# Kernel optimization log

Hardware: AMD Instinct MI355X
Metric: run time of the kernel (lower is better)

The kernel has to match this reference:

```python
import jax, jax.numpy as jnp
import numpy as np

N, CH, H, W = 2, 64, 96, 96
NH, CHUNK, RED = 4, 144, 4
CM = CH // RED  # match channels = 16
RES_SCALE = 1.0
NORM_EPS = 5e-5


def conv2d(x, w, b):
    # 3x3 'same' conv, NCHW / OIHW
    y = jax.lax.conv_general_dilated(x, w, (1, 1), 'SAME',
                                     dimension_numbers=('NCHW', 'OIHW', 'NCHW'))
    return y + b[None, :, None, None]


def setup_inputs() -> dict:
    key = jax.random.key(0)
    ks = jax.random.split(key, 8)
    L = H * W
    hb = min(L // CHUNK + (L // CHUNK) % 2, 128)  # = 64
    x = jax.random.normal(ks[0], (N, CH, H, W), jnp.float32)
    # per-round semi-orthogonal rotations: rows of (CM, hb) orthonormal
    g = jax.random.normal(ks[1], (NH, hb, CM), jnp.float32)
    q = jnp.stack([jnp.linalg.qr(g[h])[0] for h in range(NH)])  # (NH, hb, CM)
    rot = jnp.transpose(q, (2, 0, 1))  # (CM, NH, hb)
    def s(k, shape, fan):
        return jax.random.normal(k, shape, jnp.float32) / np.sqrt(fan).astype(np.float32)
    wm = s(ks[2], (CM, CH, 3, 3), CH * 9)
    wa = s(ks[3], (CH, CH, 3, 3), CH * 9)
    wf = s(ks[4], (CH, CH, 3, 3), CH * 9)
    fc1_w = s(ks[5], (CHUNK, CH), CH)
    fc2_w = s(ks[6], (CHUNK, CHUNK), CHUNK)
    return {'x': x, 'rot': rot,
            'wm': wm, 'bm': jnp.zeros((CM,), jnp.float32),
            'wa': wa, 'ba': jnp.zeros((CH,), jnp.float32),
            'wf': wf, 'bf': jnp.zeros((CH,), jnp.float32),
            'fc1_w': fc1_w, 'fc1_b': jnp.zeros((CHUNK,), jnp.float32),
            'fc2_w': fc2_w, 'fc2_b': jnp.zeros((CHUNK,), jnp.float32)}


def reference(x, rot, wm, bm, wa, ba, wf, bf, fc1_w, fc1_b, fc2_w, fc2_b):
    n, _, h, w = x.shape
    L = h * w
    hb = rot.shape[-1]
    # embeddings: (N, L, C)
    xe = jax.nn.relu(conv2d(x, wm, bm)).reshape(n, CM, L).transpose(0, 2, 1)
    ye = jax.nn.relu(conv2d(x, wa, ba)).reshape(n, CH, L).transpose(0, 2, 1)
    fe = jax.nn.relu(conv2d(x, wf, bf)).reshape(n, CH, L).transpose(0, 2, 1)
    # LSH: argmax over rotated directions, offset per round (detached in original)
    rv = jnp.einsum('ntf,fhi->nhti', xe, rot)  # (N, NH, L, hb)
    codes = jnp.argmax(rv, -1) + (jnp.arange(NH) * hb)[None, :, None]
    codes = codes.reshape(n, NH * L)
    idx = jnp.argsort(codes, axis=-1)
    undo = jnp.argsort(idx, axis=-1)
    mod = idx % L
    gather = lambda t: jnp.take_along_axis(t, mod[..., None], axis=1)
    nch = L // CHUNK  # L chosen divisible by CHUNK -> padding = 0
    xs = gather(xe).reshape(n, NH, nch, CHUNK, CM)
    ys = gather(ye).reshape(n, NH, nch, CHUNK, CH)
    fs = gather(fe).reshape(n, NH, nch, CHUNK, CH)
    nrm = jnp.linalg.norm(xs, axis=-1, keepdims=True)
    xmatch = xs / jnp.maximum(nrm, NORM_EPS)
    adj = lambda t: jnp.concatenate([t, jnp.roll(t, 1, axis=2), jnp.roll(t, -1, axis=2)], axis=3)
    xmatch = adj(xmatch)   # (n, NH, nch, 3*CHUNK, CM)
    ya = adj(ys)           # (n, NH, nch, 3*CHUNK, CH)
    fa = adj(fs)           # (n, NH, nch, 3*CHUNK, CH)
    hid = jax.nn.relu(fa @ fc1_w.T + fc1_b)
    fc_raw = jnp.swapaxes(hid @ fc2_w.T + fc2_b, -1, -2)  # (n, NH, nch, CHUNK, 3*CHUNK)
    raw = jnp.einsum('nhkie,nhkje->nhkij', xs, xmatch) + fc_raw
    bsc = jax.scipy.special.logsumexp(raw, axis=-1, keepdims=True)
    score = jnp.exp(raw - bsc)
    ret = jnp.einsum('nhkij,nhkje->nhkie', score, ya)  # (n, NH, nch, CHUNK, CH)
    ret = ret.reshape(n, NH * L, CH)
    bsc = bsc.reshape(n, NH * L)
    ret = jnp.take_along_axis(ret, undo[..., None], axis=1)
    bsc = jnp.take_along_axis(bsc, undo, axis=1)
    ret = ret.reshape(n, NH, L, CH)
    probs = jax.nn.softmax(bsc.reshape(n, NH, L, 1), axis=1)
    out = jnp.sum(ret * probs, axis=1)  # (n, L, CH)
    out = out.transpose(0, 2, 1).reshape(n, CH, h, w)
    return out * RES_SCALE + x
```

## Files before the change

kernel.cpp:

```cpp
#include <hip/hip_runtime.h>
#include <hip/hip_bf16.h>

#define LL 9216
#define TOT 36864
#define CHK 144
#define NSEG 144
#define EPS_N 5e-5f

typedef __bf16 bf16x8 __attribute__((ext_vector_type(8)));
typedef float f32x4 __attribute__((ext_vector_type(4)));

__device__ __forceinline__ float dot4(float4 a, float4 b) {
    return a.x*b.x + a.y*b.y + a.z*b.z + a.w*b.w;
}
__device__ __forceinline__ unsigned short f2bf(float f) {
    __hip_bfloat16 h = __float2bfloat16(f);
    return *reinterpret_cast<unsigned short*>(&h);
}
__device__ __forceinline__ float bf2f(unsigned short u) {
    return __uint_as_float(((unsigned int)u) << 16);
}

__global__ __launch_bounds__(256) void k_front(
    const float* __restrict__ x, const float* __restrict__ wm,
    const float* __restrict__ bm, const float* __restrict__ rot,
    unsigned short* __restrict__ xeb, unsigned short* __restrict__ xnb,
    unsigned char* __restrict__ codes,
    const float* __restrict__ fc1w, const float* __restrict__ fc2w,
    const float* __restrict__ wa, const float* __restrict__ wf,
    unsigned short* __restrict__ w1bf, unsigned short* __restrict__ w2bf,
    unsigned short* __restrict__ wpack)
{
    int tid = threadIdx.x;
    if (blockIdx.x >= 288) {
        int i = (blockIdx.x - 288) * 256 + tid;
        if (i < 144 * 64) w1bf[i] = f2bf(fc1w[i]);
        if (i < 144 * 160) {
            int r = i / 160, c = i - r * 160;
            w2bf[i] = (c < 144) ? f2bf(fc2w[r * 144 + c]) : 0;
        }
        if (i < 128 * 576) {
            int o = i / 576, kk = i - o * 576;
            int dydx = kk >> 6, c = kk & 63;
            const float* src = (o < 64) ? wa : wf;
            wpack[i] = f2bf(src[(o & 63) * 576 + c * 9 + dydx]);
        }
        return;
    }
    __shared__ float xl[6400];
    __shared__ float rotT[4096];
    __shared__ float xsp[64 * 20];
    int b = blockIdx.x;
    int n = b / 144, tile = b % 144;
    int ty0 = (tile / 12) * 8, tx0 = (tile % 12) * 8;
    for (int li = tid; li < 6400; li += 256) {
        int c = li / 100, s = li % 100;
        int yy = s / 10, xx = s % 10;
        int gy = ty0 + yy - 1, gx = tx0 + xx - 1;
        float v = 0.f;
        if ((unsigned)gy < 96u && (unsigned)gx < 96u)
            v = x[((n * 64 + c) * 96 + gy) * 96 + gx];
        xl[li] = v;
    }
    for (int e = tid; e < 4096; e += 256) {
        int f = e >> 8, r = e & 255;
        rotT[r * 16 + f] = rot[f * 256 + r];
    }
    __syncthreads();
    int p = tid & 63, og = tid >> 6;
    int row = p >> 3, col = p & 7;
    int ogs = __builtin_amdgcn_readfirstlane(og);
    const float* wb = wm + (size_t)ogs * 4 * 576;
    float acc0 = 0.f, acc1 = 0.f, acc2 = 0.f, acc3 = 0.f;
    for (int c = 0; c < 64; ++c) {
        float xp[9];
        int base = c * 100 + row * 10 + col;
        #pragma unroll
        for (int dy = 0; dy < 3; ++dy)
            #pragma unroll
            for (int dx = 0; dx < 3; ++dx)
                xp[dy * 3 + dx] = xl[base + dy * 10 + dx];
        const float* w0 = wb + c * 9;
        #pragma unroll
        for (int u = 0; u < 9; ++u) {
            acc0 += w0[u]        * xp[u];
            acc1 += w0[576 + u]  * xp[u];
            acc2 += w0[1152 + u] * xp[u];
            acc3 += w0[1728 + u] * xp[u];
        }
    }
    int o = ogs * 4;
    float v0 = acc0 + bm[o + 0]; v0 = v0 > 0.f ? v0 : 0.f;
    float v1 = acc1 + bm[o + 1]; v1 = v1 > 0.f ? v1 : 0.f;
    float v2 = acc2 + bm[o + 2]; v2 = v2 > 0.f ? v2 : 0.f;
    float v3 = acc3 + bm[o + 3]; v3 = v3 > 0.f ? v3 : 0.f;
    size_t t = (size_t)n * LL + (ty0 + row) * 96 + tx0 + col;
    unsigned short pk[4] = {f2bf(v0), f2bf(v1), f2bf(v2), f2bf(v3)};
    *(uint2*)(xeb + t * 16 + o) = *(uint2*)pk;
    *(float4*)(xsp + p * 20 + o) = make_float4(v0, v1, v2, v3);
    __syncthreads();
    int pos = tid & 63, h = tid >> 6;
    int prow = pos >> 3, pcol = pos & 7;
    size_t tc = (size_t)n * LL + (ty0 + prow) * 96 + tx0 + pcol;
    float4 q0 = *(float4*)(xsp + pos * 20 + 0);
    float4 q1 = *(float4*)(xsp + pos * 20 + 4);
    float4 q2 = *(float4*)(xsp + pos * 20 + 8);
    float4 q3 = *(float4*)(xsp + pos * 20 + 12);
    if (h == 0) {
        float nn = dot4(q0,q0) + dot4(q1,q1) + dot4(q2,q2) + dot4(q3,q3);
        float s = fmaxf(sqrtf(nn), EPS_N);
        float inv = 1.f / s;
        unsigned short pn[16];
        pn[0]=f2bf(q0.x*inv);  pn[1]=f2bf(q0.y*inv);  pn[2]=f2bf(q0.z*inv);  pn[3]=f2bf(q0.w*inv);
        pn[4]=f2bf(q1.x*inv);  pn[5]=f2bf(q1.y*inv);  pn[6]=f2bf(q1.z*inv);  pn[7]=f2bf(q1.w*inv);
        pn[8]=f2bf(q2.x*inv);  pn[9]=f2bf(q2.y*inv);  pn[10]=f2bf(q2.z*inv); pn[11]=f2bf(q2.w*inv);
        pn[12]=f2bf(q3.x*inv); pn[13]=f2bf(q3.y*inv); pn[14]=f2bf(q3.z*inv); pn[15]=f2bf(q3.w*inv);
        *(uint4*)(xnb + tc * 16)     = ((uint4*)pn)[0];
        *(uint4*)(xnb + tc * 16 + 8) = ((uint4*)pn)[1];
    }
    float best = -1e30f; int bi = 0;
    const float* rp = rotT + h * 1024;
    for (int i = 0; i < 64; ++i) {
        const float4* r4 = (const float4*)(rp + i * 16);
        float v = dot4(q0, r4[0]) + dot4(q1, r4[1]) + dot4(q2, r4[2]) + dot4(q3, r4[3]);
        if (v > best) { best = v; bi = i; }
    }
    codes[(size_t)n * TOT + h * LL + (tc - (size_t)n * LL)] = (unsigned char)(h * 64 + bi);
}

__global__ __launch_bounds__(256) void k_convbf_fc(
    const float* __restrict__ x, const unsigned short* __restrict__ wpack,
    const float* __restrict__ ba, const float* __restrict__ bfb,
    const unsigned short* __restrict__ w1bf, const float* __restrict__ fc1_b,
    const unsigned short* __restrict__ w2bf, const float* __restrict__ fc2_b,
    unsigned short* __restrict__ yeb, unsigned short* __restrict__ re2b,
    const unsigned char* __restrict__ codes, int* __restrict__ hist)
{
    __shared__ unsigned short xt[3 * 50 * 72];
    __shared__ unsigned short fet[48 * 72];
    __shared__ unsigned short hb [48 * 168];
    __shared__ int lh[256];
    int tid = threadIdx.x;
    if (blockIdx.x >= 384) {
        int b2 = blockIdx.x - 384;
        int n = b2 / NSEG, seg = b2 % NSEG;
        lh[tid] = 0;
        __syncthreads();
        int code = codes[(size_t)n * TOT + seg * 256 + tid];
        atomicAdd(&lh[code], 1);
        __syncthreads();
        hist[((size_t)n * 256 + tid) * NSEG + seg] = lh[tid];
        return;
    }
    int b = blockIdx.x;
    int n = b / 192, rem = b % 192;
    int y = rem >> 1, strip = rem & 1;
    int x0 = strip * 48;
    for (int e = tid; e < 9600; e += 256) {
        int r = e / 3200, r2 = e - r * 3200;
        int c = r2 / 50, j = r2 - c * 50;
        int gy = y - 1 + r, gx = x0 - 1 + j;
        float v = 0.f;
        if ((unsigned)gy < 96u && (unsigned)gx < 96u)
            v = x[((n * 64 + c) * 96 + gy) * 96 + gx];
        xt[(r * 50 + j) * 72 + c] = f2bf(v);
    }
    for (int e = tid; e < 384; e += 256) {
        int r = e >> 3, pq = e & 7;
        *(unsigned int*)(hb + r * 168 + 144 + pq * 2) = 0;
    }
    __syncthreads();
    int wave = tid >> 6, lane = tid & 63;
    int n16 = lane & 15, quad = lane >> 4;
    f32x4 acc[2][3];
    #pragma unroll
    for (int mi = 0; mi < 2; ++mi)
        #pragma unroll
        for (int nt = 0; nt < 3; ++nt) acc[mi][nt] = (f32x4){0.f, 0.f, 0.f, 0.f};
    #pragma unroll
    for (int s = 0; s < 18; ++s) {
        int dydx = s >> 1, half = s & 1;
        int dy = dydx / 3, dxm = dydx - dy * 3;
        bf16x8 B[3];
        #pragma unroll
        for (int nt = 0; nt < 3; ++nt) {
            int j = nt * 16 + n16 + dxm;
            B[nt] = *(bf16x8*)(xt + (dy * 50 + j) * 72 + half * 32 + quad * 8);
        }
        #pragma unroll
        for (int mi = 0; mi < 2; ++mi) {
            int o = (wave * 2 + mi) * 16 + n16;
            bf16x8 A = *(const bf16x8*)(wpack + o * 576 + dydx * 64 + half * 32 + quad * 8);
            #pragma unroll
            for (int nt = 0; nt < 3; ++nt)
                acc[mi][nt] = __builtin_amdgcn_mfma_f32_16x16x32_bf16(A, B[nt], acc[mi][nt], 0, 0, 0);
        }
    }
    #pragma unroll
    for (int mi = 0; mi < 2; ++mi) {
        int mt = wave * 2 + mi;
        int obase = mt * 16 + quad * 4;
        float4 b4 = (mt < 4) ? *(const float4*)(ba + obase)
                             : *(const float4*)(bfb + obase - 64);
        #pragma unroll
        for (int nt = 0; nt < 3; ++nt) {
            int j = nt * 16 + n16;
            unsigned short pk[4];
            float v0 = acc[mi][nt][0] + b4.x; pk[0] = f2bf(v0 > 0.f ? v0 : 0.f);
            float v1 = acc[mi][nt][1] + b4.y; pk[1] = f2bf(v1 > 0.f ? v1 : 0.f);
            float v2 = acc[mi][nt][2] + b4.z; pk[2] = f2bf(v2 > 0.f ? v2 : 0.f);
            float v3 = acc[mi][nt][3] + b4.w; pk[3] = f2bf(v3 > 0.f ? v3 : 0.f);
            if (mt < 4) {
                size_t t = (size_t)n * LL + y * 96 + x0 + j;
                *(uint2*)(yeb + t * 64 + obase) = *(uint2*)pk;
            } else {
                *(uint2*)(fet + j * 72 + (obase - 64)) = *(uint2*)pk;
            }
        }
    }
    __syncthreads();
    size_t R0 = (size_t)n * LL + y * 96 + x0;
    for (int nt = wave; nt < 9; nt += 4) {
        int bn = nt * 16 + n16;
        bf16x8 b0 = *(const bf16x8*)(w1bf + bn * 64 + quad * 8);
        bf16x8 b1 = *(const bf16x8*)(w1bf + bn * 64 + 32 + quad * 8);
        float bb = fc1_b[bn];
        #pragma unroll
        for (int m = 0; m < 3; ++m) {
            int arow = m * 16 + n16;
            bf16x8 a0 = *(bf16x8*)(fet + arow * 72 + quad * 8);
            bf16x8 a1 = *(bf16x8*)(fet + arow * 72 + 32 + quad * 8);
            f32x4 c2 = {0.f, 0.f, 0.f, 0.f};
            c2 = __builtin_amdgcn_mfma_f32_16x16x32_bf16(a0, b0, c2, 0, 0, 0);
            c2 = __builtin_amdgcn_mfma_f32_16x16x32_bf16(a1, b1, c2, 0, 0, 0);
            #pragma unroll
            for (int r = 0; r < 4; ++r) {
                float v = c2[r] + bb;
                hb[(m * 16 + quad * 4 + r) * 168 + bn] = f2bf(v > 0.f ? v : 0.f);
            }
        }
    }
    __syncthreads();
    for (int nt = wave; nt < 9; nt += 4) {
        int bn = nt * 16 + n16;
        bf16x8 wv2[5];
        #pragma unroll
        for (int kk = 0; kk < 5; ++kk)
            wv2[kk] = *(const bf16x8*)(w2bf + bn * 160 + kk * 32 + quad * 8);
        float bb = fc2_b[bn];
        #pragma unroll
        for (int m = 0; m < 3; ++m) {
            int arow = m * 16 + n16;
            f32x4 c2 = {0.f, 0.f, 0.f, 0.f};
            #pragma unroll
            for (int kk = 0; kk < 5; ++kk) {
                bf16x8 a = *(bf16x8*)(hb + arow * 168 + kk * 32 + quad * 8);
                c2 = __builtin_amdgcn_mfma_f32_16x16x32_bf16(a, wv2[kk], c2, 0, 0, 0);
            }
            #pragma unroll
            for (int r = 0; r < 4; ++r)
                re2b[(R0 + m * 16 + quad * 4 + r) * 144 + bn] = f2bf(c2[r] + bb);
        }
    }
}

__global__ void k_scan(int* __restrict__ hist)
{
    __shared__ int sc[256];
    int n = blockIdx.x, bin = threadIdx.x;
    int* hp = hist + ((size_t)n * 256 + bin) * NSEG;
    int4 buf[36];
    int4* hp4 = (int4*)hp;
    #pragma unroll
    for (int q = 0; q < 36; ++q) buf[q] = hp4[q];
    int running = 0;
    #pragma unroll
    for (int q = 0; q < 36; ++q) {
        int t0 = buf[q].x; buf[q].x = running; running += t0;
        int t1 = buf[q].y; buf[q].y = running; running += t1;
        int t2 = buf[q].z; buf[q].z = running; running += t2;
        int t3 = buf[q].w; buf[q].w = running; running += t3;
    }
    sc[bin] = running;
    __syncthreads();
    for (int off = 1; off < 256; off <<= 1) {
        int v = sc[bin];
        int u = (bin >= off) ? sc[bin - off] : 0;
        __syncthreads();
        sc[bin] = v + u;
        __syncthreads();
    }
    int bs = sc[bin] - running;
    #pragma unroll
    for (int q = 0; q < 36; ++q) {
        buf[q].x += bs; buf[q].y += bs; buf[q].z += bs; buf[q].w += bs;
        hp4[q] = buf[q];
    }
}

__global__ __launch_bounds__(256) void k_place(
    const unsigned char* __restrict__ codes, const int* __restrict__ hist,
    int* __restrict__ idx)
{
    __shared__ unsigned char cl[256];
    int b = blockIdx.x, n = b / NSEG, seg = b % NSEG;
    int tid = threadIdx.x;
    int my = codes[(size_t)n * TOT + seg * 256 + tid];
    cl[tid] = (unsigned char)my;
    __syncthreads();
    int rank = 0;
    for (int j = 0; j < tid; ++j) rank += (cl[j] == my);
    int pos = hist[((size_t)n * 256 + my) * NSEG + seg] + rank;
    idx[(size_t)n * TOT + pos] = seg * 256 + tid;
}

__global__ __launch_bounds__(256) void k_gather(
    const int* __restrict__ idx, const unsigned short* __restrict__ xeb,
    const unsigned short* __restrict__ xnb, const unsigned short* __restrict__ yeb,
    const unsigned short* __restrict__ re2b,
    unsigned short* __restrict__ qs, unsigned short* __restrict__ ks,
    unsigned short* __restrict__ vsT, unsigned short* __restrict__ fst,
    int* __restrict__ undo)
{
    __shared__ int tl[144];
    int b0 = blockIdx.x;
    int b = ((b0 & 7) << 6) | (b0 >> 3);
    int nh = b >> 6, chunk = b & 63;
    int n = nh >> 2, h = nh & 3;
    size_t gb = (size_t)nh * LL + chunk * 144;
    size_t nL = (size_t)n * LL;
    int tid = threadIdx.x;
    if (tid < 144) {
        int t = idx[(size_t)n * TOT + h * LL + chunk * 144 + tid] - h * LL;
        tl[tid] = t;
        undo[(size_t)nh * LL + t] = chunk * 144 + tid;
    }
    __syncthreads();
    for (int e = tid; e < 288; e += 256) {
        int s = e >> 1, half = e & 1;
        size_t src = (nL + tl[s]) * 16 + half * 8;
        *(uint4*)(qs + (gb + s) * 16 + half * 8) = *(const uint4*)(xeb + src);
        *(uint4*)(ks + (gb + s) * 16 + half * 8) = *(const uint4*)(xnb + src);
    }
    size_t vb = (size_t)(nh * 64 + chunk) * 64;
    for (int e = tid; e < 576; e += 256) {
        int p = e % 72, su = e / 72;
        uint4 a  = *(const uint4*)(yeb + (nL + tl[2 * p])     * 64 + su * 8);
        uint4 bq = *(const uint4*)(yeb + (nL + tl[2 * p + 1]) * 64 + su * 8);
        const unsigned short* pa = (const unsigned short*)&a;
        const unsigned short* pb = (const unsigned short*)&bq;
        #pragma unroll
        for (int ci = 0; ci < 8; ++ci) {
            int c = su * 8 + ci;
            *(unsigned int*)(vsT + (vb + c) * 144 + 2 * p) =
                (unsigned int)pa[ci] | ((unsigned int)pb[ci] << 16);
        }
    }
    for (int e = tid; e < 1296; e += 256) {
        int mt = e / 144, s = e - mt * 144;
        const unsigned short* src = re2b + (nL + tl[s]) * 144 + mt * 16;
        unsigned short* dst = fst + ((size_t)(nh * 9 + mt) * LL + chunk * 144 + s) * 16;
        *(uint4*)(dst)     = *(const uint4*)(src);
        *(uint4*)(dst + 8) = *(const uint4*)(src + 8);
    }
}

__global__ __launch_bounds__(576, 4) void k_attn(
    const unsigned short* __restrict__ qs, const unsigned short* __restrict__ ks,
    const unsigned short* __restrict__ vsT, const unsigned short* __restrict__ fst,
    unsigned short* __restrict__ rets, float* __restrict__ bscs)
{
    __shared__ __align__(16) unsigned short Pw[9][16 * 56];

    int B = blockIdx.x;
    int bucket = ((B & 7) << 6) | (B >> 3);
    int n = bucket >> 8, rem = bucket & 255;
    int h = rem >> 6, k = rem & 63;
    int nh = n * 4 + h;
    int tid = threadIdx.x;
    int lane = tid & 63, mt = tid >> 6;
    int n16 = lane & 15, quad = lane >> 4;

    size_t hL = (size_t)nh * LL;
    int ch0 = k, ch1 = (k + 63) & 63, ch2 = (k + 1) & 63;
    unsigned short* Pp = &Pw[mt][0];
    const unsigned short* fsl = fst + (size_t)(nh * 9 + mt) * LL * 16;

    bf16x8 afragQ = {};
    if (quad < 2)
        afragQ = *(const bf16x8*)(qs + (hL + ch0 * 144 + mt * 16 + n16) * 16 + quad * 8);

    f32x4 acc[4];
    float rm[4], rl[4];
    #pragma unroll
    for (int ct = 0; ct < 4; ++ct) acc[ct] = (f32x4){0.f, 0.f, 0.f, 0.f};
    #pragma unroll
    for (int r = 0; r < 4; ++r) { rm[r] = -1e30f; rl[r] = 0.f; }

    #pragma unroll
    for (int reg = 0; reg < 3; ++reg) {
        int chx = (reg == 0) ? ch0 : ((reg == 1) ? ch1 : ch2);
        int cb = chx * 144;
        const unsigned short* vchunk = vsT + (size_t)(nh * 64 + chx) * 64 * 144;
        #pragma unroll
        for (int sub = 0; sub < 3; ++sub) {
            int sl = cb + sub * 48;
            bf16x8 ksf[3] = {};
            if (quad < 2) {
                ksf[0] = *(const bf16x8*)(ks + (hL + sl + n16) * 16 + quad * 8);
                ksf[1] = *(const bf16x8*)(ks + (hL + sl + 16 + n16) * 16 + quad * 8);
                ksf[2] = *(const bf16x8*)(ks + (hL + sl + 32 + n16) * 16 + quad * 8);
            }
            ushort4 fv[3];
            #pragma unroll
            for (int nt = 0; nt < 3; ++nt)
                fv[nt] = *(const ushort4*)(fsl + (size_t)(sl + nt * 16 + n16) * 16 + quad * 4);
            f32x4 c0 = {bf2f(fv[0].x), bf2f(fv[0].y), bf2f(fv[0].z), bf2f(fv[0].w)};
            f32x4 c1 = {bf2f(fv[1].x), bf2f(fv[1].y), bf2f(fv[1].z), bf2f(fv[1].w)};
            f32x4 c2 = {bf2f(fv[2].x), bf2f(fv[2].y), bf2f(fv[2].z), bf2f(fv[2].w)};
            c0 = __builtin_amdgcn_mfma_f32_16x16x32_bf16(afragQ, ksf[0], c0, 0, 0, 0);
            c1 = __builtin_amdgcn_mfma_f32_16x16x32_bf16(afragQ, ksf[1], c1, 0, 0, 0);
            c2 = __builtin_amdgcn_mfma_f32_16x16x32_bf16(afragQ, ksf[2], c2, 0, 0, 0);
            #pragma unroll
            for (int r = 0; r < 4; ++r) {
                float v0 = c0[r], v1 = c1[r], v2 = c2[r];
                float mm = fmaxf(fmaxf(v0, v1), v2);
                mm = fmaxf(mm, __shfl_xor(mm, 1, 16));
                mm = fmaxf(mm, __shfl_xor(mm, 2, 16));
                mm = fmaxf(mm, __shfl_xor(mm, 4, 16));
                mm = fmaxf(mm, __shfl_xor(mm, 8, 16));
                float mn = fmaxf(rm[r], mm);
                float a = __expf(rm[r] - mn);
                float s0 = __expf(v0 - mn), s1 = __expf(v1 - mn), s2 = __expf(v2 - mn);
                float ss = s0 + s1 + s2;
                ss += __shfl_xor(ss, 1, 16);
                ss += __shfl_xor(ss, 2, 16);
                ss += __shfl_xor(ss, 4, 16);
                ss += __shfl_xor(ss, 8, 16);
                rl[r] = rl[r] * a + ss;
                rm[r] = mn;
                acc[0][r] *= a; acc[1][r] *= a; acc[2][r] *= a; acc[3][r] *= a;
                int rw = quad * 4 + r;
                Pp[rw * 56 +      n16] = f2bf(s0);
                Pp[rw * 56 + 16 + n16] = f2bf(s1);
                Pp[rw * 56 + 32 + n16] = f2bf(s2);
            }
            #pragma unroll
            for (int kk = 0; kk < 2; ++kk) {
                int koff = (kk == 0) ? (quad * 8) : (quad < 2 ? 32 + quad * 8 : 0);
                bf16x8 Bv[4];
                #pragma unroll
                for (int ct = 0; ct < 4; ++ct)
                    Bv[ct] = *(const bf16x8*)(vchunk
                        + (size_t)(ct * 16 + n16) * 144 + sub * 48 + koff);
                bf16x8 Ap = {};
                if (kk == 0)
                    Ap = *(const bf16x8*)(Pp + n16 * 56 + quad * 8);
                else if (quad < 2)
                    Ap = *(const bf16x8*)(Pp + n16 * 56 + 32 + quad * 8);
                #pragma unroll
                for (int ct = 0; ct < 4; ++ct)
                    acc[ct] = __builtin_amdgcn_mfma_f32_16x16x32_bf16(Ap, Bv[ct], acc[ct], 0, 0, 0);
            }
        }
    }

    size_t sp0 = hL + ch0 * 144;
    if (n16 == 0) {
        #pragma unroll
        for (int r = 0; r < 4; ++r)
            bscs[sp0 + mt * 16 + quad * 4 + r] = rm[r] + __logf(rl[r]);
    }
    #pragma unroll
    for (int r = 0; r < 4; ++r) {
        float inv = 1.f / rl[r];
        #pragma unroll
        for (int ct = 0; ct < 4; ++ct)
            rets[(sp0 + mt * 16 + quad * 4 + r) * 64 + ct * 16 + n16] =
                f2bf(acc[ct][r] * inv);
    }
}

__global__ __launch_bounds__(256) void k_final(
    const unsigned short* __restrict__ rets, const float* __restrict__ bscs,
    const int* __restrict__ undo, const float* __restrict__ x,
    float* __restrict__ out)
{
    __shared__ float pr[4][64];
    __shared__ int us[4][64];
    __shared__ float accl[64 * 65];
    int b = blockIdx.x, n = b / 144;
    int t0 = (b % 144) * 64;
    int tid = threadIdx.x;
    {
        int h = tid >> 6, tt = tid & 63;
        us[h][tt] = undo[((size_t)n * 4 + h) * LL + t0 + tt];
    }
    __syncthreads();
    if (tid < 64) {
        float b0 = bscs[((size_t)n * 4 + 0) * LL + us[0][tid]];
        float b1 = bscs[((size_t)n * 4 + 1) * LL + us[1][tid]];
        float b2 = bscs[((size_t)n * 4 + 2) * LL + us[2][tid]];
        float b3 = bscs[((size_t)n * 4 + 3) * LL + us[3][tid]];
        float mx = fmaxf(fmaxf(b0, b1), fmaxf(b2, b3));
        float e0 = __expf(b0-mx), e1 = __expf(b1-mx), e2 = __expf(b2-mx), e3 = __expf(b3-mx);
        float inv = 1.f / (e0 + e1 + e2 + e3);
        pr[0][tid] = e0*inv; pr[1][tid] = e1*inv; pr[2][tid] = e2*inv; pr[3][tid] = e3*inv;
    }
    __syncthreads();
    int cc = tid & 63, tt4 = tid >> 6;
    #pragma unroll
    for (int q = 0; q < 16; ++q) {
        int tt = tt4 + 4*q;
        float v = 0.f;
        #pragma unroll
        for (int h2 = 0; h2 < 4; ++h2)
            v += bf2f(rets[(((size_t)n*4 + h2)*LL + us[h2][tt])*64 + cc]) * pr[h2][tt];
        accl[cc*65 + tt] = v;
    }
    __syncthreads();
    int tt = tid & 63, c4 = tid >> 6;
    #pragma unroll
    for (int q = 0; q < 16; ++q) {
        int ch = c4 + 4*q;
        size_t o = ((size_t)n*64 + ch)*LL + t0 + tt;
        out[o] = accl[ch*65 + tt] + x[o];
    }
}

extern "C" void kernel_launch(void* const* d_in, const int* in_sizes, int n_in,
                              void* d_out, int out_size, void* d_ws, size_t ws_size,
                              hipStream_t stream)
{
    const float* x    = (const float*)d_in[0];
    const float* rot  = (const float*)d_in[1];
    const float* wm   = (const float*)d_in[2];
    const float* bm   = (const float*)d_in[3];
    const float* wa   = (const float*)d_in[4];
    const float* ba   = (const float*)d_in[5];
    const float* wf   = (const float*)d_in[6];
    const float* bf   = (const float*)d_in[7];
    const float* fc1w = (const float*)d_in[8];
    const float* fc1b = (const float*)d_in[9];
    const float* fc2w = (const float*)d_in[10];
    const float* fc2b = (const float*)d_in[11];
    float* out = (float*)d_out;

    char* ws = (char*)d_ws;
    unsigned short* xeb  = (unsigned short*)(ws + 0);
    unsigned short* yeb  = (unsigned short*)(ws + 589824);
    unsigned short* xnb  = (unsigned short*)(ws + 2949120);
    unsigned short* re2b = (unsigned short*)(ws + 3538944);
    unsigned short* w1bf = (unsigned short*)(ws + 8847360);
    unsigned short* w2bf = (unsigned short*)(ws + 8865792);
    unsigned short* wpak = (unsigned short*)(ws + 8911872);
    unsigned char* codes = (unsigned char*)(ws + 9059328);
    int* hist            = (int*)(ws + 9133056);
    int* idxb            = (int*)(ws + 9427968);
    unsigned short* rets = (unsigned short*)(ws + 0);
    float* bscs          = (float*)(ws + 9437184);
    unsigned short* qs   = (unsigned short*)(ws + 9732096);
    unsigned short* ks   = (unsigned short*)(ws + 12091392);
    unsigned short* vsT  = (unsigned short*)(ws + 14450688);
    unsigned short* fst  = (unsigned short*)(ws + 23887872);
    int* undo            = (int*)(ws + 45121536);

    k_front    <<<576, 256, 0, stream>>>(x, wm, bm, rot, xeb, xnb, codes,
                                         fc1w, fc2w, wa, wf, w1bf, w2bf, wpak);
    k_convbf_fc<<<672, 256, 0, stream>>>(x, wpak, ba, bf, w1bf, fc1b, w2bf, fc2b,
                                         yeb, re2b, codes, hist);
    k_scan     <<<2,    256, 0, stream>>>(hist);
    k_place    <<<288,  256, 0, stream>>>(codes, hist, idxb);
    k_gather   <<<512,  256, 0, stream>>>(idxb, xeb, xnb, yeb, re2b,
                                          qs, ks, vsT, fst, undo);
    k_attn     <<<512,  576, 0, stream>>>(qs, ks, vsT, fst, rets, bscs);
    k_final    <<<288,  256, 0, stream>>>(rets, bscs, undo, x, out);
}
```

Before: 236.3 us.

## Software-pipeline K/F and V loads in attention loop with double buffering

Unrolls the nine attention sub-iterations by hand and prefetches the next iteration's key and fc-bias fragments into alternate register buffers while the current one computes. V fragments for the first half of the PV product are loaded before the softmax, so their global-load latency overlaps the score computation. This adds register pressure from the doubled buffers, which could reduce occupancy.

```diff
diff --git a/kernel.cpp b/kernel.cpp
--- a/kernel.cpp
+++ b/kernel.cpp
@@ -397,73 +397,93 @@
     #pragma unroll
     for (int r = 0; r < 4; ++r) { rm[r] = -1e30f; rl[r] = 0.f; }
 
-    #pragma unroll
-    for (int reg = 0; reg < 3; ++reg) {
-        int chx = (reg == 0) ? ch0 : ((reg == 1) ? ch1 : ch2);
-        int cb = chx * 144;
-        const unsigned short* vchunk = vsT + (size_t)(nh * 64 + chx) * 64 * 144;
-        #pragma unroll
-        for (int sub = 0; sub < 3; ++sub) {
-            int sl = cb + sub * 48;
-            bf16x8 ksf[3] = {};
-            if (quad < 2) {
-                ksf[0] = *(const bf16x8*)(ks + (hL + sl + n16) * 16 + quad * 8);
-                ksf[1] = *(const bf16x8*)(ks + (hL + sl + 16 + n16) * 16 + quad * 8);
-                ksf[2] = *(const bf16x8*)(ks + (hL + sl + 32 + n16) * 16 + quad * 8);
-            }
-            ushort4 fv[3];
-            #pragma unroll
-            for (int nt = 0; nt < 3; ++nt)
-                fv[nt] = *(const ushort4*)(fsl + (size_t)(sl + nt * 16 + n16) * 16 + quad * 4);
-            f32x4 c0 = {bf2f(fv[0].x), bf2f(fv[0].y), bf2f(fv[0].z), bf2f(fv[0].w)};
-            f32x4 c1 = {bf2f(fv[1].x), bf2f(fv[1].y), bf2f(fv[1].z), bf2f(fv[1].w)};
-            f32x4 c2 = {bf2f(fv[2].x), bf2f(fv[2].y), bf2f(fv[2].z), bf2f(fv[2].w)};
-            c0 = __builtin_amdgcn_mfma_f32_16x16x32_bf16(afragQ, ksf[0], c0, 0, 0, 0);
-            c1 = __builtin_amdgcn_mfma_f32_16x16x32_bf16(afragQ, ksf[1], c1, 0, 0, 0);
-            c2 = __builtin_amdgcn_mfma_f32_16x16x32_bf16(afragQ, ksf[2], c2, 0, 0, 0);
-            #pragma unroll
-            for (int r = 0; r < 4; ++r) {
-                float v0 = c0[r], v1 = c1[r], v2 = c2[r];
-                float mm = fmaxf(fmaxf(v0, v1), v2);
-                mm = fmaxf(mm, __shfl_xor(mm, 1, 16));
-                mm = fmaxf(mm, __shfl_xor(mm, 2, 16));
-                mm = fmaxf(mm, __shfl_xor(mm, 4, 16));
-                mm = fmaxf(mm, __shfl_xor(mm, 8, 16));
-                float mn = fmaxf(rm[r], mm);
-                float a = __expf(rm[r] - mn);
-                float s0 = __expf(v0 - mn), s1 = __expf(v1 - mn), s2 = __expf(v2 - mn);
-                float ss = s0 + s1 + s2;
-                ss += __shfl_xor(ss, 1, 16);
-                ss += __shfl_xor(ss, 2, 16);
-                ss += __shfl_xor(ss, 4, 16);
-                ss += __shfl_xor(ss, 8, 16);
-                rl[r] = rl[r] * a + ss;
-                rm[r] = mn;
-                acc[0][r] *= a; acc[1][r] *= a; acc[2][r] *= a; acc[3][r] *= a;
-                int rw = quad * 4 + r;
-                Pp[rw * 56 +      n16] = f2bf(s0);
-                Pp[rw * 56 + 16 + n16] = f2bf(s1);
-                Pp[rw * 56 + 32 + n16] = f2bf(s2);
-            }
-            #pragma unroll
-            for (int kk = 0; kk < 2; ++kk) {
-                int koff = (kk == 0) ? (quad * 8) : (quad < 2 ? 32 + quad * 8 : 0);
-                bf16x8 Bv[4];
-                #pragma unroll
-                for (int ct = 0; ct < 4; ++ct)
-                    Bv[ct] = *(const bf16x8*)(vchunk
-                        + (size_t)(ct * 16 + n16) * 144 + sub * 48 + koff);
-                bf16x8 Ap = {};
-                if (kk == 0)
-                    Ap = *(const bf16x8*)(Pp + n16 * 56 + quad * 8);
-                else if (quad < 2)
-                    Ap = *(const bf16x8*)(Pp + n16 * 56 + 32 + quad * 8);
-                #pragma unroll
-                for (int ct = 0; ct < 4; ++ct)
-                    acc[ct] = __builtin_amdgcn_mfma_f32_16x16x32_bf16(Ap, Bv[ct], acc[ct], 0, 0, 0);
-            }
-        }
-    }
+#define SLOT(T) ((((T) < 3) ? ch0 : ((T) < 6) ? ch1 : ch2) * 144 + ((T) % 3) * 48)
+
+#define LOAD_KF(T, KS, FV) do {                                                      \
+    int sl_ = SLOT(T);                                                               \
+    if (quad < 2) {                                                                  \
+        KS[0] = *(const bf16x8*)(ks + (hL + sl_ + n16) * 16 + quad * 8);             \
+        KS[1] = *(const bf16x8*)(ks + (hL + sl_ + 16 + n16) * 16 + quad * 8);        \
+        KS[2] = *(const bf16x8*)(ks + (hL + sl_ + 32 + n16) * 16 + quad * 8);        \
+    }                                                                                \
+    FV[0] = *(const ushort4*)(fsl + (size_t)(sl_ + n16) * 16 + quad * 4);            \
+    FV[1] = *(const ushort4*)(fsl + (size_t)(sl_ + 16 + n16) * 16 + quad * 4);       \
+    FV[2] = *(const ushort4*)(fsl + (size_t)(sl_ + 32 + n16) * 16 + quad * 4);       \
+} while (0)
+
+#define ATTN_ITER(T, KS, FV, NKS, NFV) do {                                          \
+    int chx_ = ((T) < 3) ? ch0 : ((T) < 6) ? ch1 : ch2;                              \
+    const unsigned short* vch_ = vsT + (size_t)(nh * 64 + chx_) * 9216;              \
+    int vo_ = ((T) % 3) * 48;                                                        \
+    bf16x8 Bv0_[4];                                                                  \
+    _Pragma("unroll")                                                                \
+    for (int ct_ = 0; ct_ < 4; ++ct_)                                                \
+        Bv0_[ct_] = *(const bf16x8*)(vch_ + (size_t)(ct_ * 16 + n16) * 144 + vo_ + quad * 8); \
+    if ((T) < 8) LOAD_KF((T) + 1, NKS, NFV);                                         \
+    f32x4 c0_ = {bf2f(FV[0].x), bf2f(FV[0].y), bf2f(FV[0].z), bf2f(FV[0].w)};        \
+    f32x4 c1_ = {bf2f(FV[1].x), bf2f(FV[1].y), bf2f(FV[1].z), bf2f(FV[1].w)};        \
+    f32x4 c2_ = {bf2f(FV[2].x), bf2f(FV[2].y), bf2f(FV[2].z), bf2f(FV[2].w)};        \
+    c0_ = __builtin_amdgcn_mfma_f32_16x16x32_bf16(afragQ, KS[0], c0_, 0, 0, 0);      \
+    c1_ = __builtin_amdgcn_mfma_f32_16x16x32_bf16(afragQ, KS[1], c1_, 0, 0, 0);      \
+    c2_ = __builtin_amdgcn_mfma_f32_16x16x32_bf16(afragQ, KS[2], c2_, 0, 0, 0);      \
+    _Pragma("unroll")                                                                \
+    for (int r_ = 0; r_ < 4; ++r_) {                                                 \
+        float v0_ = c0_[r_], v1_ = c1_[r_], v2_ = c2_[r_];                           \
+        float mm_ = fmaxf(fmaxf(v0_, v1_), v2_);                                     \
+        mm_ = fmaxf(mm_, __shfl_xor(mm_, 1, 16));                                    \
+        mm_ = fmaxf(mm_, __shfl_xor(mm_, 2, 16));                                    \
+        mm_ = fmaxf(mm_, __shfl_xor(mm_, 4, 16));                                    \
+        mm_ = fmaxf(mm_, __shfl_xor(mm_, 8, 16));                                    \
+        float mn_ = fmaxf(rm[r_], mm_);                                              \
+        float a_ = __expf(rm[r_] - mn_);                                             \
+        float s0_ = __expf(v0_ - mn_), s1_ = __expf(v1_ - mn_), s2_ = __expf(v2_ - mn_); \
+        float ss_ = s0_ + s1_ + s2_;                                                 \
+        ss_ += __shfl_xor(ss_, 1, 16);                                               \
+        ss_ += __shfl_xor(ss_, 2, 16);                                               \
+        ss_ += __shfl_xor(ss_, 4, 16);                                               \
+        ss_ += __shfl_xor(ss_, 8, 16);                                               \
+        rl[r_] = rl[r_] * a_ + ss_;                                                  \
+        rm[r_] = mn_;                                                                \
+        acc[0][r_] *= a_; acc[1][r_] *= a_; acc[2][r_] *= a_; acc[3][r_] *= a_;      \
+        int rw_ = quad * 4 + r_;                                                     \
+        Pp[rw_ * 56 +      n16] = f2bf(s0_);                                         \
+        Pp[rw_ * 56 + 16 + n16] = f2bf(s1_);                                         \
+        Pp[rw_ * 56 + 32 + n16] = f2bf(s2_);                                         \
+    }                                                                                \
+                \
+    bf16x8 Ap0_ = *(const bf16x8*)(Pp + n16 * 56 + quad * 8);                        \
+    int ko1_ = (quad < 2) ? 32 + quad * 8 : 0;          \
+    bf16x8 Bv1_[4];                                                                  \
+    _Pragma("unroll")                                                                \
+    for (int ct_ = 0; ct_ < 4; ++ct_)                                                \
+        Bv1_[ct_] = *(const bf16x8*)(vch_ + (size_t)(ct_ * 16 + n16) * 144 + vo_ + ko1_); \
+    _Pragma("unroll")                                                                \
+    for (int ct_ = 0; ct_ < 4; ++ct_)                                                \
+        acc[ct_] = __builtin_amdgcn_mfma_f32_16x16x32_bf16(Ap0_, Bv0_[ct_], acc[ct_], 0, 0, 0); \
+    bf16x8 Ap1_ = {};                                                                \
+    if (quad < 2)                                                                    \
+        Ap1_ = *(const bf16x8*)(Pp + n16 * 56 + 32 + quad * 8);                      \
+    _Pragma("unroll")                                                                \
+    for (int ct_ = 0; ct_ < 4; ++ct_)                                                \
+        acc[ct_] = __builtin_amdgcn_mfma_f32_16x16x32_bf16(Ap1_, Bv1_[ct_], acc[ct_], 0, 0, 0); \
+} while (0)
+
+    bf16x8 ksA[3] = {}, ksB[3] = {};
+    ushort4 fvA[3], fvB[3];
+    LOAD_KF(0, ksA, fvA);
+    ATTN_ITER(0, ksA, fvA, ksB, fvB);
+    ATTN_ITER(1, ksB, fvB, ksA, fvA);
+    ATTN_ITER(2, ksA, fvA, ksB, fvB);
+    ATTN_ITER(3, ksB, fvB, ksA, fvA);
+    ATTN_ITER(4, ksA, fvA, ksB, fvB);
+    ATTN_ITER(5, ksB, fvB, ksA, fvA);
+    ATTN_ITER(6, ksA, fvA, ksB, fvB);
+    ATTN_ITER(7, ksB, fvB, ksA, fvA);
+    ATTN_ITER(8, ksA, fvA, ksB, fvB);
+
+#undef ATTN_ITER
+#undef LOAD_KF
+#undef SLOT
 
     size_t sp0 = hL + ch0 * 144;
     if (n16 == 0) {
```

Result: slower. 276.1 us (+16.8%).
